# Kernel tuning notes

Hardware: AMD Instinct MI355X
Metric: run time of the kernel (lower is better)

Reference implementation:

```python
import jax, jax.numpy as jnp
import numpy as np

B, C, H, W = 2, 64, 270, 480
CQ = C // 8


def _distance_weight(n):
    i = jnp.arange(n, dtype=jnp.float32)
    d = i[None, :] - i[:, None]  # j - i
    return jnp.exp(-(d * d) / (2.0 * (n * n / 4.0)))  # [n, n]


def setup_inputs() -> dict:
    key = jax.random.key(0)
    ks = jax.random.split(key, 8)
    s = 0.05
    return {
        "x": jax.random.normal(ks[0], (B, C, H, W), jnp.float32),
        "Wq": jax.random.normal(ks[1], (CQ, C), jnp.float32) * s,
        "bq": jax.random.normal(ks[2], (CQ,), jnp.float32) * s,
        "Wk": jax.random.normal(ks[3], (CQ, C), jnp.float32) * s,
        "bk": jax.random.normal(ks[4], (CQ,), jnp.float32) * s,
        "Wv": jax.random.normal(ks[5], (C, C), jnp.float32) * s,
        "bv": jax.random.normal(ks[6], (C,), jnp.float32) * s,
        "gamma": jax.random.normal(ks[7], (), jnp.float32) * 0.3,
        "dw_h": _distance_weight(H),  # [H, H] non-trainable buffer
        "dw_w": _distance_weight(W),  # [W, W] non-trainable buffer
    }


def reference(x, Wq, bq, Wk, bk, Wv, bv, gamma, dw_h, dw_w):
    # 1x1 convs == per-pixel linear projections
    q = jnp.einsum('oc,bchw->bohw', Wq, x) + bq[None, :, None, None]  # [B,CQ,H,W]
    k = jnp.einsum('oc,bchw->bohw', Wk, x) + bk[None, :, None, None]  # [B,CQ,H,W]
    v = jnp.einsum('oc,bchw->bohw', Wv, x) + bv[None, :, None, None]  # [B,C,H,W]

    height, width = x.shape[2], x.shape[3]
    neg_inf = jnp.float32(-jnp.inf)

    # row (H-direction) energy: queries/keys along the height axis per column w
    e_h = jnp.einsum('bchw,bcgw->bwhg', q, k) * dw_h[None, None]  # [B,W,H,H]
    # diagonal -inf mask (dw_h diag == 1, so order of mul is immaterial)
    eye_h = jnp.eye(height, dtype=bool)
    e_h = jnp.where(eye_h[None, None], neg_inf, e_h)
    e_h = jnp.transpose(e_h, (0, 2, 1, 3))  # [B,H,W,H]

    # column (W-direction) energy along the width axis per row h
    e_w = jnp.einsum('bchw,bchv->bhwv', q, k) * dw_w[None, None]  # [B,H,W,W]

    # joint softmax over concatenated H and W directions
    att = jax.nn.softmax(jnp.concatenate([e_h, e_w], axis=3), axis=3)  # [B,H,W,H+W]
    att_h = jnp.transpose(att[:, :, :, :height], (0, 2, 1, 3))  # [B,W,H,H]
    att_w = att[:, :, :, height:]  # [B,H,W,W]

    out_h = jnp.einsum('bcgw,bwhg->bchw', v, att_h)  # [B,C,H,W]
    out_w = jnp.einsum('bchv,bhwv->bchw', v, att_w)  # [B,C,H,W]

    return gamma * (out_h + out_w) + x
```

## Files before the change

### kernel.cpp

```cpp
#include <hip/hip_runtime.h>
#include <hip/hip_bf16.h>

namespace {

constexpr int B  = 2;
constexpr int C  = 64;
constexpr int CQ = 8;
constexpr int H  = 270;
constexpr int W  = 480;
constexpr int HW = H * W;
constexpr float INVH2 = 2.0f / (270.0f * 270.0f);
constexpr float INVW2 = 2.0f / (480.0f * 480.0f);

typedef __attribute__((ext_vector_type(4))) float f32x4;
typedef __attribute__((ext_vector_type(8))) short short8;
typedef __attribute__((ext_vector_type(4))) unsigned int uint4v;

__device__ __forceinline__ float bits2f(unsigned short u) {
  union { unsigned int i; float f; } cv;
  cv.i = ((unsigned int)u) << 16;
  return cv.f;
}

__device__ __forceinline__ unsigned short f2bf(float f) {
  union { __hip_bfloat16 b; unsigned short u; } cv;
  cv.b = __float2bfloat16(f);
  return cv.u;
}

__device__ __forceinline__ unsigned int pack2(float a, float b) {
  return ((unsigned int)f2bf(b) << 16) | (unsigned int)f2bf(a);
}

__device__ __forceinline__ short8 pack_p(const float p0[4], const float p1[4]) {
  uint4v pw;
  pw[0] = pack2(p0[0], p0[1]);
  pw[1] = pack2(p0[2], p0[3]);
  pw[2] = pack2(p1[0], p1[1]);
  pw[3] = pack2(p1[2], p1[3]);
  return __builtin_bit_cast(short8, pw);
}


__global__ __launch_bounds__(256, 1)
void k_qkv(const float* __restrict__ x,
           const float* __restrict__ Wq, const float* __restrict__ bq,
           const float* __restrict__ Wk, const float* __restrict__ bk,
           const float* __restrict__ Wv, const float* __restrict__ bv,
           unsigned short* __restrict__ qwp, unsigned short* __restrict__ kwp,
           unsigned short* __restrict__ qhp, unsigned short* __restrict__ khp,
           unsigned short* __restrict__ v, unsigned short* __restrict__ vt) {
  __shared__ __align__(16) float wql[CQ * C];
  __shared__ __align__(16) float wkl[CQ * C];
  __shared__ __align__(16) float wvl[C * C];
  __shared__ float bql[CQ], bkl[CQ], bvl[C];
  const int tid = threadIdx.x;
  for (int i = tid; i < CQ * C; i += 256) { wql[i] = Wq[i]; wkl[i] = Wk[i]; }
  for (int i = tid; i < C * C; i += 256) wvl[i] = Wv[i];
  if (tid < CQ) { bql[tid] = bq[tid]; bkl[tid] = bk[tid]; }
  if (tid < C) bvl[tid] = bv[tid];
  __syncthreads();
  const int pix0 = (blockIdx.x * 256 + tid) * 2;
  if (pix0 >= B * HW) return;
  const int b = pix0 / HW;
  const int r = pix0 - b * HW;
  const int h = r / W;
  const int w = r - h * W;

  float qa0[CQ], qa1[CQ], ka0[CQ], ka1[CQ], va0[C], va1[C];
#pragma unroll
  for (int o = 0; o < CQ; ++o) {
    qa0[o] = bql[o]; qa1[o] = bql[o];
    ka0[o] = bkl[o]; ka1[o] = bkl[o];
  }
#pragma unroll
  for (int o = 0; o < C; ++o) { va0[o] = bvl[o]; va1[o] = bvl[o]; }

  const float* xp = x + (size_t)b * C * HW + r;
  for (int c = 0; c < C; c += 4) {
    const float2 x0 = *(const float2*)(xp + (size_t)(c + 0) * HW);
    const float2 x1 = *(const float2*)(xp + (size_t)(c + 1) * HW);
    const float2 x2 = *(const float2*)(xp + (size_t)(c + 2) * HW);
    const float2 x3 = *(const float2*)(xp + (size_t)(c + 3) * HW);
#pragma unroll
    for (int o = 0; o < CQ; ++o) {
      const float4 a = *(const float4*)(wql + o * C + c);
      qa0[o] = fmaf(a.w, x3.x, fmaf(a.z, x2.x, fmaf(a.y, x1.x, fmaf(a.x, x0.x, qa0[o]))));
      qa1[o] = fmaf(a.w, x3.y, fmaf(a.z, x2.y, fmaf(a.y, x1.y, fmaf(a.x, x0.y, qa1[o]))));
      const float4 bb = *(const float4*)(wkl + o * C + c);
      ka0[o] = fmaf(bb.w, x3.x, fmaf(bb.z, x2.x, fmaf(bb.y, x1.x, fmaf(bb.x, x0.x, ka0[o]))));
      ka1[o] = fmaf(bb.w, x3.y, fmaf(bb.z, x2.y, fmaf(bb.y, x1.y, fmaf(bb.x, x0.y, ka1[o]))));
    }
#pragma unroll
    for (int o = 0; o < C; ++o) {
      const float4 cc = *(const float4*)(wvl + o * C + c);
      va0[o] = fmaf(cc.w, x3.x, fmaf(cc.z, x2.x, fmaf(cc.y, x1.x, fmaf(cc.x, x0.x, va0[o]))));
      va1[o] = fmaf(cc.w, x3.y, fmaf(cc.z, x2.y, fmaf(cc.y, x1.y, fmaf(cc.x, x0.y, va1[o]))));
    }
  }

  uint4 qp0, kp0, qp1, kp1;
  qp0.x = pack2(qa0[0], qa0[1]); qp0.y = pack2(qa0[2], qa0[3]);
  qp0.z = pack2(qa0[4], qa0[5]); qp0.w = pack2(qa0[6], qa0[7]);
  kp0.x = pack2(ka0[0], ka0[1]); kp0.y = pack2(ka0[2], ka0[3]);
  kp0.z = pack2(ka0[4], ka0[5]); kp0.w = pack2(ka0[6], ka0[7]);
  qp1.x = pack2(qa1[0], qa1[1]); qp1.y = pack2(qa1[2], qa1[3]);
  qp1.z = pack2(qa1[4], qa1[5]); qp1.w = pack2(qa1[6], qa1[7]);
  kp1.x = pack2(ka1[0], ka1[1]); kp1.y = pack2(ka1[2], ka1[3]);
  kp1.z = pack2(ka1[4], ka1[5]); kp1.w = pack2(ka1[6], ka1[7]);
  *(uint4*)(qwp + (size_t)pix0 * 8) = qp0;
  *(uint4*)(qwp + (size_t)(pix0 + 1) * 8) = qp1;
  *(uint4*)(kwp + (size_t)pix0 * 8) = kp0;
  *(uint4*)(kwp + (size_t)(pix0 + 1) * 8) = kp1;
  const size_t tb0 = ((size_t)b * W + w) * H + h;
  const size_t tb1 = tb0 + H;
  *(uint4*)(qhp + tb0 * 8) = qp0;
  *(uint4*)(qhp + tb1 * 8) = qp1;
  *(uint4*)(khp + tb0 * 8) = kp0;
  *(uint4*)(khp + tb1 * 8) = kp1;

  unsigned short* vp = v + (size_t)b * C * HW + r;
#pragma unroll
  for (int o = 0; o < C; ++o)
    *(unsigned int*)(vp + (size_t)o * HW) = pack2(va0[o], va1[o]);
  unsigned short* vt0 = vt + tb0 * C;
  unsigned short* vt1 = vt + tb1 * C;
#pragma unroll
  for (int j = 0; j < 16; ++j) {
    ushort4 u0, u1;
    u0.x = f2bf(va0[4 * j + 0]); u0.y = f2bf(va0[4 * j + 1]);
    u0.z = f2bf(va0[4 * j + 2]); u0.w = f2bf(va0[4 * j + 3]);
    u1.x = f2bf(va1[4 * j + 0]); u1.y = f2bf(va1[4 * j + 1]);
    u1.z = f2bf(va1[4 * j + 2]); u1.w = f2bf(va1[4 * j + 3]);
    *(ushort4*)(vt0 + 4 * j) = u0;
    *(ushort4*)(vt1 + 4 * j) = u1;
  }
}

constexpr int VSW = 494;

__global__ __launch_bounds__(512, 1)
void k_outw(const unsigned short* __restrict__ qwp,
            const unsigned short* __restrict__ kwp,
            const unsigned short* __restrict__ v,
            unsigned short* __restrict__ ow, float* __restrict__ Sw) {
  __shared__ __align__(16) unsigned short vbs[64 * VSW];
  __shared__ __align__(16) unsigned short kls[480 * 8];
  const int h = blockIdx.x >> 1, z = blockIdx.x & 1;
  const int b = blockIdx.y;
  const int tid = threadIdx.x;
  const size_t rowbase = ((size_t)b * H + h) * W;

  const unsigned short* vrow = v + (size_t)b * C * HW + (size_t)h * W;
  ushort4 vr0[8];
#pragma unroll
  for (int it = 0; it < 8; ++it) {
    const int idx = tid + it * 512;
    const int c = idx / 120, s4 = (idx - c * 120) * 4;
    vr0[it] = *(const ushort4*)(vrow + (size_t)c * HW + s4);
  }
  uint4 kreg;
  if (tid < 480) kreg = *(const uint4*)(kwp + (rowbase + tid) * 8);
#pragma unroll
  for (int it = 0; it < 8; ++it) {
    const int idx = tid + it * 512;
    const int c = idx / 120, s4 = (idx - c * 120) * 4;
    const int u = s4 & 31;
    const int t = (u < 16) ? ((u >> 2) * 8) : (((u - 16) >> 2) * 8 + 4);
    *(ushort4*)(vbs + c * VSW + (s4 & ~31) + t) = vr0[it];
  }
  ushort4 vr1[7];
#pragma unroll
  for (int it = 0; it < 7; ++it) {
    const int idx = tid + (8 + it) * 512;
    const int c = idx / 120, s4 = (idx - c * 120) * 4;
    vr1[it] = *(const ushort4*)(vrow + (size_t)c * HW + s4);
  }
#pragma unroll
  for (int it = 0; it < 7; ++it) {
    const int idx = tid + (8 + it) * 512;
    const int c = idx / 120, s4 = (idx - c * 120) * 4;
    const int u = s4 & 31;
    const int t = (u < 16) ? ((u >> 2) * 8) : (((u - 16) >> 2) * 8 + 4);
    *(ushort4*)(vbs + c * VSW + (s4 & ~31) + t) = vr1[it];
  }
  if (tid < 480) *(uint4*)(kls + tid * 8) = kreg;

  const int lane = tid & 63, wv = tid >> 6;
  const int l15 = lane & 15, quad = lane >> 4;
  const int chunk = z * 8 + wv;
  const bool active = chunk < 15;
  const int m0 = chunk * 32;

  short8 qa0 = short8{0, 0, 0, 0, 0, 0, 0, 0};
  short8 qa1 = short8{0, 0, 0, 0, 0, 0, 0, 0};
  if (quad == 0 && active) {
    qa0 = *(const short8*)(qwp + (rowbase + m0 + l15) * 8);
    qa1 = *(const short8*)(qwp + (rowbase + m0 + 16 + l15) * 8);
  }

  f32x4 acc[2][4];
  float Sacc[2] = {0.0f, 0.0f};
#pragma unroll
  for (int mt = 0; mt < 2; ++mt)
#pragma unroll
    for (int ct = 0; ct < 4; ++ct)
#pragma unroll
      for (int rr = 0; rr < 4; ++rr) acc[mt][ct][rr] = 0.0f;

  __syncthreads();

  if (active) {
    short8 kb0 = short8{0, 0, 0, 0, 0, 0, 0, 0};
    short8 kb1 = short8{0, 0, 0, 0, 0, 0, 0, 0};
    if (quad == 0) {
      kb0 = *(const short8*)(kls + (l15) * 8);
      kb1 = *(const short8*)(kls + (16 + l15) * 8);
    }
    for (int ci = 0; ci < 15; ++ci) {
      const int sc = ci * 32;
      short8 nk0 = short8{0, 0, 0, 0, 0, 0, 0, 0};
      short8 nk1 = short8{0, 0, 0, 0, 0, 0, 0, 0};
      if (ci < 14 && quad == 0) {
        nk0 = *(const short8*)(kls + (sc + 32 + l15) * 8);
        nk1 = *(const short8*)(kls + (sc + 48 + l15) * 8);
      }
      short8 vb[4];
#pragma unroll
      for (int ct = 0; ct < 4; ++ct)
        vb[ct] = *(const short8*)(vbs + (ct * 16 + l15) * VSW + sc + quad * 8);
      const f32x4 z4 = f32x4{0.f, 0.f, 0.f, 0.f};
      const f32x4 E00 = __builtin_amdgcn_mfma_f32_16x16x32_bf16(kb0, qa0, z4, 0, 0, 0);
      const f32x4 E01 = __builtin_amdgcn_mfma_f32_16x16x32_bf16(kb1, qa0, z4, 0, 0, 0);
      const f32x4 E10 = __builtin_amdgcn_mfma_f32_16x16x32_bf16(kb0, qa1, z4, 0, 0, 0);
      const f32x4 E11 = __builtin_amdgcn_mfma_f32_16x16x32_bf16(kb1, qa1, z4, 0, 0, 0);
#pragma unroll
      for (int mt = 0; mt < 2; ++mt) {
        const int m = m0 + mt * 16 + l15;
        const f32x4 Ea = mt ? E10 : E00;
        const f32x4 Eb = mt ? E11 : E01;
        float p0[4], p1[4];
#pragma unroll
        for (int rr = 0; rr < 4; ++rr) {
          const float d0 = (float)(m - (sc + quad * 4 + rr));
          const float d1 = d0 - 16.0f;
          p0[rr] = __expf(Ea[rr] * __expf(-(d0 * d0) * INVW2));
          p1[rr] = __expf(Eb[rr] * __expf(-(d1 * d1) * INVW2));
          Sacc[mt] += p0[rr] + p1[rr];
        }
        const short8 pa = pack_p(p0, p1);
#pragma unroll
        for (int ct = 0; ct < 4; ++ct)
          acc[mt][ct] = __builtin_amdgcn_mfma_f32_16x16x32_bf16(pa, vb[ct], acc[mt][ct], 0, 0, 0);
      }
      kb0 = nk0;
      kb1 = nk1;
    }

#pragma unroll
    for (int mt = 0; mt < 2; ++mt) {
      float s = Sacc[mt];
      s += __shfl_xor(s, 16);
      s += __shfl_xor(s, 32);
      if (lane < 16) Sw[rowbase + m0 + mt * 16 + l15] = s;
    }
  }

  __syncthreads();
  unsigned short* ob = vbs;
  if (active) {
#pragma unroll
    for (int mt = 0; mt < 2; ++mt)
#pragma unroll
      for (int ct = 0; ct < 4; ++ct)
#pragma unroll
        for (int rr = 0; rr < 4; ++rr)
          ob[(ct * 16 + l15) * VSW + m0 + mt * 16 + quad * 4 + rr] = f2bf(acc[mt][ct][rr]);
  }
  __syncthreads();
  unsigned short* og = ow + ((size_t)b * H + h) * C * W;
  const int mlo = z ? 256 : 0;
  const int nu = z ? 112 : 128;
  for (int idx = tid; idx < 64 * nu; idx += 512) {
    const int c = idx / nu, i = idx - c * nu;
    *(unsigned int*)(og + (size_t)c * W + mlo + 2 * i) =
        *(const unsigned int*)(ob + c * VSW + mlo + 2 * i);
  }
}

constexpr int VSH = 302;

__global__ __launch_bounds__(576, 1)
void k_outh(const unsigned short* __restrict__ qhp,
            const unsigned short* __restrict__ khp,
            const unsigned short* __restrict__ vt,
            unsigned short* __restrict__ oht, float* __restrict__ Sht) {
  __shared__ __align__(16) unsigned short vbs[64 * VSH];
  __shared__ __align__(16) unsigned short kls[288 * 8];
  const int w = blockIdx.x >> 1, z = blockIdx.x & 1;
  const int b = blockIdx.y;
  const int tid = threadIdx.x;
  const size_t colbase = ((size_t)b * W + w) * H;

  const unsigned short* vtb = vt + colbase * C;
  ushort4 vreg[8];
#pragma unroll
  for (int it = 0; it < 8; ++it) {
    const int idx = tid + it * 576;
    const int g = idx >> 4, c4 = (idx & 15) * 4;
    vreg[it] = (g < H) ? *(const ushort4*)(vtb + (size_t)g * C + c4)
                       : make_ushort4(0, 0, 0, 0);
  }
  uint4 kreg;
  if (tid < 288) kreg = *(const uint4*)(khp + (colbase + min(tid, H - 1)) * 8);
#pragma unroll
  for (int it = 0; it < 8; ++it) {
    const int idx = tid + it * 576;
    const int g = idx >> 4, c4 = (idx & 15) * 4;
    const int u = g & 31;
    const int t = (u < 16) ? ((u >> 2) * 8 + (u & 3))
                           : (((u - 16) >> 2) * 8 + 4 + (u & 3));
    const int slot = (g & ~31) + t;
    vbs[(c4 + 0) * VSH + slot] = vreg[it].x;
    vbs[(c4 + 1) * VSH + slot] = vreg[it].y;
    vbs[(c4 + 2) * VSH + slot] = vreg[it].z;
    vbs[(c4 + 3) * VSH + slot] = vreg[it].w;
  }
  if (tid < 288) *(uint4*)(kls + tid * 8) = kreg;

  const int lane = tid & 63, wv = tid >> 6;
  const int l15 = lane & 15, quad = lane >> 4;
  const int m0 = (z * 9 + wv) * 16;
  const int m = m0 + l15;

  short8 qa = short8{0, 0, 0, 0, 0, 0, 0, 0};
  if (quad == 0)
    qa = *(const short8*)(qhp + (colbase + min(m, H - 1)) * 8);

  f32x4 acc[4];
  float Sacc = 0.0f;
#pragma unroll
  for (int ct = 0; ct < 4; ++ct)
#pragma unroll
    for (int rr = 0; rr < 4; ++rr) acc[ct][rr] = 0.0f;

  __syncthreads();

  for (int ci = 0; ci < 9; ++ci) {
    const int gc = ci * 32;
    short8 kb0 = short8{0, 0, 0, 0, 0, 0, 0, 0};
    short8 kb1 = short8{0, 0, 0, 0, 0, 0, 0, 0};
    if (quad == 0) {
      kb0 = *(const short8*)(kls + (gc + l15) * 8);
      kb1 = *(const short8*)(kls + (gc + 16 + l15) * 8);
    }
    short8 vb[4];
#pragma unroll
    for (int ct = 0; ct < 4; ++ct)
      vb[ct] = *(const short8*)(vbs + (ct * 16 + l15) * VSH + gc + quad * 8);
    const f32x4 z4 = f32x4{0.f, 0.f, 0.f, 0.f};
    const f32x4 E0 = __builtin_amdgcn_mfma_f32_16x16x32_bf16(kb0, qa, z4, 0, 0, 0);
    const f32x4 E1 = __builtin_amdgcn_mfma_f32_16x16x32_bf16(kb1, qa, z4, 0, 0, 0);
    float p0[4], p1[4];
#pragma unroll
    for (int rr = 0; rr < 4; ++rr) {
      const int g0 = gc + quad * 4 + rr;
      const int g1 = g0 + 16;
      const float d0 = (float)(m - g0);
      const float d1 = d0 - 16.0f;
      p0[rr] = (g0 < H && g0 != m)
                   ? __expf(E0[rr] * __expf(-(d0 * d0) * INVH2)) : 0.0f;
      p1[rr] = (g1 < H && g1 != m)
                   ? __expf(E1[rr] * __expf(-(d1 * d1) * INVH2)) : 0.0f;
      Sacc += p0[rr] + p1[rr];
    }
    const short8 pa = pack_p(p0, p1);
#pragma unroll
    for (int ct = 0; ct < 4; ++ct)
      acc[ct] = __builtin_amdgcn_mfma_f32_16x16x32_bf16(pa, vb[ct], acc[ct], 0, 0, 0);
  }

  {
    float s = Sacc;
    s += __shfl_xor(s, 16);
    s += __shfl_xor(s, 32);
    if (lane < 16 && m < H) Sht[colbase + m] = s;
  }

  __syncthreads();
  unsigned short* ob = vbs;
#pragma unroll
  for (int ct = 0; ct < 4; ++ct)
#pragma unroll
    for (int rr = 0; rr < 4; ++rr)
      ob[(ct * 16 + l15) * VSH + m0 + quad * 4 + rr] = f2bf(acc[ct][rr]);
  __syncthreads();
  unsigned short* og = oht + ((size_t)b * W + w) * C * H;
  const int mlo = z ? 144 : 0;
  const int nu = z ? 63 : 72;
  for (int idx = tid; idx < 64 * nu; idx += 576) {
    const int c = idx / nu, i = idx - c * nu;
    *(unsigned int*)(og + (size_t)c * H + mlo + 2 * i) =
        *(const unsigned int*)(ob + c * VSH + mlo + 2 * i);
  }
}

__global__ __launch_bounds__(256)
void k_combine(const unsigned short* __restrict__ oht,
               const unsigned short* __restrict__ ow,
               const float* __restrict__ Sht, const float* __restrict__ Sw,
               const float* __restrict__ x,
               const float* __restrict__ gp,
               float* __restrict__ out) {
  __shared__ float tile[32][33];
  const int b = blockIdx.z >> 6, c = blockIdx.z & 63;
  const int w0 = blockIdx.x * 32, h0 = blockIdx.y * 32;
  const int tx = threadIdx.x, ty = threadIdx.y;
#pragma unroll
  for (int i = 0; i < 4; ++i) {
    const int wl = ty + i * 8;
    const int hh = h0 + tx;
    float val = 0.0f;
    if (hh < H) val = bits2f(oht[(((size_t)b * W + (w0 + wl)) * C + c) * H + hh]);
    tile[wl][tx] = val;
  }
  __syncthreads();
  const float gamma = *gp;
#pragma unroll
  for (int i = 0; i < 4; ++i) {
    const int hl = ty + i * 8;
    const int hh = h0 + hl;
    if (hh < H) {
      const int ww = w0 + tx;
      const float uh = tile[tx][hl];
      const float uw = bits2f(ow[(((size_t)b * H + hh) * C + c) * W + ww]);
      const size_t si = ((size_t)b * H + hh) * W + ww;
      const float Z = Sht[((size_t)b * W + ww) * H + hh] + Sw[si];
      const float invZ = __builtin_amdgcn_rcpf(Z);
      const size_t xi = ((size_t)b * C + c) * HW + (size_t)hh * W + ww;
      out[xi] = fmaf(gamma * invZ, uh + uw, x[xi]);
    }
  }
}

}

extern "C" void kernel_launch(void* const* d_in, const int* in_sizes, int n_in,
                              void* d_out, int out_size, void* d_ws, size_t ws_size,
                              hipStream_t stream) {
  (void)in_sizes; (void)n_in; (void)out_size; (void)ws_size;
  const float* x  = (const float*)d_in[0];
  const float* Wq = (const float*)d_in[1];
  const float* bq = (const float*)d_in[2];
  const float* Wk = (const float*)d_in[3];
  const float* bk = (const float*)d_in[4];
  const float* Wv = (const float*)d_in[5];
  const float* bv = (const float*)d_in[6];
  const float* gp = (const float*)d_in[7];
  float* out = (float*)d_out;

  char* p = (char*)d_ws;
  auto take = [&](size_t bytes) -> void* {
    char* r = p;
    p += (bytes + 255) & ~(size_t)255;
    return (void*)r;
  };
  unsigned short* qwp = (unsigned short*)take(sizeof(unsigned short) * (size_t)B * HW * 8);
  unsigned short* kwp = (unsigned short*)take(sizeof(unsigned short) * (size_t)B * HW * 8);
  unsigned short* qhp = (unsigned short*)take(sizeof(unsigned short) * (size_t)B * HW * 8);
  unsigned short* khp = (unsigned short*)take(sizeof(unsigned short) * (size_t)B * HW * 8);
  unsigned short* v   = (unsigned short*)take(sizeof(unsigned short) * (size_t)B * C * HW);
  unsigned short* vt  = (unsigned short*)take(sizeof(unsigned short) * (size_t)B * C * HW);
  unsigned short* oht = (unsigned short*)take(sizeof(unsigned short) * (size_t)B * C * HW);
  unsigned short* owb = (unsigned short*)take(sizeof(unsigned short) * (size_t)B * C * HW);
  float* Sht = (float*)take(sizeof(float) * (size_t)B * HW);
  float* Sw  = (float*)take(sizeof(float) * (size_t)B * HW);

  hipLaunchKernelGGL(k_qkv, dim3((B * HW / 2 + 255) / 256), dim3(256), 0, stream,
                     x, Wq, bq, Wk, bk, Wv, bv, qwp, kwp, qhp, khp, v, vt);
  hipLaunchKernelGGL(k_outh, dim3(2 * W, B), dim3(576), 0, stream,
                     qhp, khp, vt, oht, Sht);
  hipLaunchKernelGGL(k_outw, dim3(2 * H, B), dim3(512), 0, stream,
                     qwp, kwp, v, owb, Sw);
  hipLaunchKernelGGL(k_combine, dim3(W / 32, (H + 31) / 32, B * C), dim3(32, 8), 0, stream,
                     oht, owb, Sht, Sw, x, gp, out);
}
```

Baseline: 398.8 us.

## Fuse H- and W-direction attention kernels into one launch with interleaved blocks

Merges the separate k_outh and k_outw kernels into a single 640-thread kernel whose grid interleaves row-attention and column-attention blocks. W-direction rows are now split into three blocks of 160 queries, with one 16-query tile per wave instead of two. H-direction columns use 10 waves per half. This removes a kernel boundary and lets the two workloads overlap and balance across CUs. In exchange, both paths now share one shared-memory allocation and one register budget, the W path loses its two-tile K reuse and K prefetch, and some H-path waves sit idle.

New measurement: 516.8 us. 1.3x slower.

```diff
diff --git a/kernel.cpp b/kernel.cpp
--- a/kernel.cpp
+++ b/kernel.cpp
@@ -138,270 +138,248 @@
 }
 
 constexpr int VSW = 494;
-
-__global__ __launch_bounds__(512, 1)
-void k_outw(const unsigned short* __restrict__ qwp,
-            const unsigned short* __restrict__ kwp,
-            const unsigned short* __restrict__ v,
-            unsigned short* __restrict__ ow, float* __restrict__ Sw) {
-  __shared__ __align__(16) unsigned short vbs[64 * VSW];
-  __shared__ __align__(16) unsigned short kls[480 * 8];
-  const int h = blockIdx.x >> 1, z = blockIdx.x & 1;
+constexpr int VSH = 302;
+
+__global__ __launch_bounds__(640, 1)
+void k_att(const unsigned short* __restrict__ qwp,
+           const unsigned short* __restrict__ kwp,
+           const unsigned short* __restrict__ v,
+           unsigned short* __restrict__ ow, float* __restrict__ Sw,
+           const unsigned short* __restrict__ qhp,
+           const unsigned short* __restrict__ khp,
+           const unsigned short* __restrict__ vt,
+           unsigned short* __restrict__ oht, float* __restrict__ Sht) {
+  __shared__ __align__(16) unsigned short smem[64 * VSW + 480 * 8];
   const int b = blockIdx.y;
   const int tid = threadIdx.x;
-  const size_t rowbase = ((size_t)b * H + h) * W;
-
-  const unsigned short* vrow = v + (size_t)b * C * HW + (size_t)h * W;
-  ushort4 vr0[8];
-#pragma unroll
-  for (int it = 0; it < 8; ++it) {
-    const int idx = tid + it * 512;
-    const int c = idx / 120, s4 = (idx - c * 120) * 4;
-    vr0[it] = *(const ushort4*)(vrow + (size_t)c * HW + s4);
-  }
-  uint4 kreg;
-  if (tid < 480) kreg = *(const uint4*)(kwp + (rowbase + tid) * 8);
-#pragma unroll
-  for (int it = 0; it < 8; ++it) {
-    const int idx = tid + it * 512;
-    const int c = idx / 120, s4 = (idx - c * 120) * 4;
-    const int u = s4 & 31;
-    const int t = (u < 16) ? ((u >> 2) * 8) : (((u - 16) >> 2) * 8 + 4);
-    *(ushort4*)(vbs + c * VSW + (s4 & ~31) + t) = vr0[it];
-  }
-  ushort4 vr1[7];
-#pragma unroll
-  for (int it = 0; it < 7; ++it) {
-    const int idx = tid + (8 + it) * 512;
-    const int c = idx / 120, s4 = (idx - c * 120) * 4;
-    vr1[it] = *(const ushort4*)(vrow + (size_t)c * HW + s4);
-  }
-#pragma unroll
-  for (int it = 0; it < 7; ++it) {
-    const int idx = tid + (8 + it) * 512;
-    const int c = idx / 120, s4 = (idx - c * 120) * 4;
-    const int u = s4 & 31;
-    const int t = (u < 16) ? ((u >> 2) * 8) : (((u - 16) >> 2) * 8 + 4);
-    *(ushort4*)(vbs + c * VSW + (s4 & ~31) + t) = vr1[it];
-  }
-  if (tid < 480) *(uint4*)(kls + tid * 8) = kreg;
-
   const int lane = tid & 63, wv = tid >> 6;
   const int l15 = lane & 15, quad = lane >> 4;
-  const int chunk = z * 8 + wv;
-  const bool active = chunk < 15;
-  const int m0 = chunk * 32;
-
-  short8 qa0 = short8{0, 0, 0, 0, 0, 0, 0, 0};
-  short8 qa1 = short8{0, 0, 0, 0, 0, 0, 0, 0};
-  if (quad == 0 && active) {
-    qa0 = *(const short8*)(qwp + (rowbase + m0 + l15) * 8);
-    qa1 = *(const short8*)(qwp + (rowbase + m0 + 16 + l15) * 8);
-  }
-
-  f32x4 acc[2][4];
-  float Sacc[2] = {0.0f, 0.0f};
-#pragma unroll
-  for (int mt = 0; mt < 2; ++mt)
+
+  const int i = blockIdx.x;
+  int part, j;
+  if (i < 1620) { part = i & 1; j = i >> 1; }
+  else          { part = 0;     j = 810 + (i - 1620); }
+
+  if (part == 1) {
+    const int h = j / 3, zz = j - (j / 3) * 3;
+    unsigned short* vbs = smem;
+    unsigned short* kls = smem + 64 * VSW;
+    const size_t rowbase = ((size_t)b * H + h) * W;
+    const unsigned short* vrow = v + (size_t)b * C * HW + (size_t)h * W;
+
+    ushort4 vr[6];
+#pragma unroll
+    for (int it = 0; it < 6; ++it) {
+      const int idx = tid + it * 640;
+      const int c = idx / 120, s4 = (idx - c * 120) * 4;
+      vr[it] = *(const ushort4*)(vrow + (size_t)c * HW + s4);
+    }
+    uint4 kreg;
+    if (tid < 480) kreg = *(const uint4*)(kwp + (rowbase + tid) * 8);
+#pragma unroll
+    for (int it = 0; it < 6; ++it) {
+      const int idx = tid + it * 640;
+      const int c = idx / 120, s4 = (idx - c * 120) * 4;
+      const int u = s4 & 31;
+      const int t = (u < 16) ? ((u >> 2) * 8) : (((u - 16) >> 2) * 8 + 4);
+      *(ushort4*)(vbs + c * VSW + (s4 & ~31) + t) = vr[it];
+    }
+#pragma unroll
+    for (int it = 0; it < 6; ++it) {
+      const int idx = tid + (6 + it) * 640;
+      const int c = idx / 120, s4 = (idx - c * 120) * 4;
+      vr[it] = *(const ushort4*)(vrow + (size_t)c * HW + s4);
+    }
+#pragma unroll
+    for (int it = 0; it < 6; ++it) {
+      const int idx = tid + (6 + it) * 640;
+      const int c = idx / 120, s4 = (idx - c * 120) * 4;
+      const int u = s4 & 31;
+      const int t = (u < 16) ? ((u >> 2) * 8) : (((u - 16) >> 2) * 8 + 4);
+      *(ushort4*)(vbs + c * VSW + (s4 & ~31) + t) = vr[it];
+    }
+    if (tid < 480) *(uint4*)(kls + tid * 8) = kreg;
+
+    const int m0 = (zz * 10 + wv) * 16;
+    const int m = m0 + l15;
+
+    short8 qa = short8{0, 0, 0, 0, 0, 0, 0, 0};
+    if (quad == 0) qa = *(const short8*)(qwp + (rowbase + m) * 8);
+
+    f32x4 acc[4];
+    float Sacc = 0.0f;
 #pragma unroll
     for (int ct = 0; ct < 4; ++ct)
 #pragma unroll
-      for (int rr = 0; rr < 4; ++rr) acc[mt][ct][rr] = 0.0f;
-
-  __syncthreads();
-
-  if (active) {
-    short8 kb0 = short8{0, 0, 0, 0, 0, 0, 0, 0};
-    short8 kb1 = short8{0, 0, 0, 0, 0, 0, 0, 0};
-    if (quad == 0) {
-      kb0 = *(const short8*)(kls + (l15) * 8);
-      kb1 = *(const short8*)(kls + (16 + l15) * 8);
-    }
+      for (int rr = 0; rr < 4; ++rr) acc[ct][rr] = 0.0f;
+
+    __syncthreads();
+
     for (int ci = 0; ci < 15; ++ci) {
       const int sc = ci * 32;
-      short8 nk0 = short8{0, 0, 0, 0, 0, 0, 0, 0};
-      short8 nk1 = short8{0, 0, 0, 0, 0, 0, 0, 0};
-      if (ci < 14 && quad == 0) {
-        nk0 = *(const short8*)(kls + (sc + 32 + l15) * 8);
-        nk1 = *(const short8*)(kls + (sc + 48 + l15) * 8);
+      short8 kb0 = short8{0, 0, 0, 0, 0, 0, 0, 0};
+      short8 kb1 = short8{0, 0, 0, 0, 0, 0, 0, 0};
+      if (quad == 0) {
+        kb0 = *(const short8*)(kls + (sc + l15) * 8);
+        kb1 = *(const short8*)(kls + (sc + 16 + l15) * 8);
       }
       short8 vb[4];
 #pragma unroll
       for (int ct = 0; ct < 4; ++ct)
         vb[ct] = *(const short8*)(vbs + (ct * 16 + l15) * VSW + sc + quad * 8);
       const f32x4 z4 = f32x4{0.f, 0.f, 0.f, 0.f};
-      const f32x4 E00 = __builtin_amdgcn_mfma_f32_16x16x32_bf16(kb0, qa0, z4, 0, 0, 0);
-      const f32x4 E01 = __builtin_amdgcn_mfma_f32_16x16x32_bf16(kb1, qa0, z4, 0, 0, 0);
-      const f32x4 E10 = __builtin_amdgcn_mfma_f32_16x16x32_bf16(kb0, qa1, z4, 0, 0, 0);
-      const f32x4 E11 = __builtin_amdgcn_mfma_f32_16x16x32_bf16(kb1, qa1, z4, 0, 0, 0);
-#pragma unroll
-      for (int mt = 0; mt < 2; ++mt) {
-        const int m = m0 + mt * 16 + l15;
-        const f32x4 Ea = mt ? E10 : E00;
-        const f32x4 Eb = mt ? E11 : E01;
+      const f32x4 E0 = __builtin_amdgcn_mfma_f32_16x16x32_bf16(kb0, qa, z4, 0, 0, 0);
+      const f32x4 E1 = __builtin_amdgcn_mfma_f32_16x16x32_bf16(kb1, qa, z4, 0, 0, 0);
+      float p0[4], p1[4];
+#pragma unroll
+      for (int rr = 0; rr < 4; ++rr) {
+        const float d0 = (float)(m - (sc + quad * 4 + rr));
+        const float d1 = d0 - 16.0f;
+        p0[rr] = __expf(E0[rr] * __expf(-(d0 * d0) * INVW2));
+        p1[rr] = __expf(E1[rr] * __expf(-(d1 * d1) * INVW2));
+        Sacc += p0[rr] + p1[rr];
+      }
+      const short8 pa = pack_p(p0, p1);
+#pragma unroll
+      for (int ct = 0; ct < 4; ++ct)
+        acc[ct] = __builtin_amdgcn_mfma_f32_16x16x32_bf16(pa, vb[ct], acc[ct], 0, 0, 0);
+    }
+
+    {
+      float s = Sacc;
+      s += __shfl_xor(s, 16);
+      s += __shfl_xor(s, 32);
+      if (lane < 16) Sw[rowbase + m] = s;
+    }
+
+    __syncthreads();
+    unsigned short* ob = vbs;
+#pragma unroll
+    for (int ct = 0; ct < 4; ++ct)
+#pragma unroll
+      for (int rr = 0; rr < 4; ++rr)
+        ob[(ct * 16 + l15) * VSW + m0 + quad * 4 + rr] = f2bf(acc[ct][rr]);
+    __syncthreads();
+    unsigned short* og = ow + ((size_t)b * H + h) * C * W;
+    const int mlo = zz * 160;
+    for (int idx = tid; idx < 64 * 80; idx += 640) {
+      const int c = idx / 80, i2 = idx - c * 80;
+      *(unsigned int*)(og + (size_t)c * W + mlo + 2 * i2) =
+          *(const unsigned int*)(ob + c * VSW + mlo + 2 * i2);
+    }
+  } else {
+    const int w = j >> 1, z = j & 1;
+    unsigned short* vbs = smem;
+    unsigned short* kls = smem + 64 * VSH;
+    const size_t colbase = ((size_t)b * W + w) * H;
+    const unsigned short* vtb = vt + colbase * C;
+
+    ushort4 vreg[8];
+#pragma unroll
+    for (int it = 0; it < 8; ++it) {
+      const int idx = tid + it * 640;
+      if (idx < 4608) {
+        const int g = idx >> 4, c4 = (idx & 15) * 4;
+        vreg[it] = (g < H) ? *(const ushort4*)(vtb + (size_t)g * C + c4)
+                           : make_ushort4(0, 0, 0, 0);
+      }
+    }
+    uint4 kreg;
+    if (tid < 288) kreg = *(const uint4*)(khp + (colbase + min(tid, H - 1)) * 8);
+#pragma unroll
+    for (int it = 0; it < 8; ++it) {
+      const int idx = tid + it * 640;
+      if (idx < 4608) {
+        const int g = idx >> 4, c4 = (idx & 15) * 4;
+        const int u = g & 31;
+        const int t = (u < 16) ? ((u >> 2) * 8 + (u & 3))
+                               : (((u - 16) >> 2) * 8 + 4 + (u & 3));
+        const int slot = (g & ~31) + t;
+        vbs[(c4 + 0) * VSH + slot] = vreg[it].x;
+        vbs[(c4 + 1) * VSH + slot] = vreg[it].y;
+        vbs[(c4 + 2) * VSH + slot] = vreg[it].z;
+        vbs[(c4 + 3) * VSH + slot] = vreg[it].w;
+      }
+    }
+    if (tid < 288) *(uint4*)(kls + tid * 8) = kreg;
+
+    const int chunk = z * 10 + wv;
+    const bool active = chunk < 18;
+    const int m0 = chunk * 16;
+    const int m = m0 + l15;
+
+    short8 qa = short8{0, 0, 0, 0, 0, 0, 0, 0};
+    if (quad == 0 && active)
+      qa = *(const short8*)(qhp + (colbase + min(m, H - 1)) * 8);
+
+    f32x4 acc[4];
+    float Sacc = 0.0f;
+#pragma unroll
+    for (int ct = 0; ct < 4; ++ct)
+#pragma unroll
+      for (int rr = 0; rr < 4; ++rr) acc[ct][rr] = 0.0f;
+
+    __syncthreads();
+
+    if (active) {
+      for (int ci = 0; ci < 9; ++ci) {
+        const int gc = ci * 32;
+        short8 kb0 = short8{0, 0, 0, 0, 0, 0, 0, 0};
+        short8 kb1 = short8{0, 0, 0, 0, 0, 0, 0, 0};
+        if (quad == 0) {
+          kb0 = *(const short8*)(kls + (gc + l15) * 8);
+          kb1 = *(const short8*)(kls + (gc + 16 + l15) * 8);
+        }
+        short8 vb[4];
+#pragma unroll
+        for (int ct = 0; ct < 4; ++ct)
+          vb[ct] = *(const short8*)(vbs + (ct * 16 + l15) * VSH + gc + quad * 8);
+        const f32x4 z4 = f32x4{0.f, 0.f, 0.f, 0.f};
+        const f32x4 E0 = __builtin_amdgcn_mfma_f32_16x16x32_bf16(kb0, qa, z4, 0, 0, 0);
+        const f32x4 E1 = __builtin_amdgcn_mfma_f32_16x16x32_bf16(kb1, qa, z4, 0, 0, 0);
         float p0[4], p1[4];
 #pragma unroll
         for (int rr = 0; rr < 4; ++rr) {
-          const float d0 = (float)(m - (sc + quad * 4 + rr));
+          const int g0 = gc + quad * 4 + rr;
+          const int g1 = g0 + 16;
+          const float d0 = (float)(m - g0);
           const float d1 = d0 - 16.0f;
-          p0[rr] = __expf(Ea[rr] * __expf(-(d0 * d0) * INVW2));
-          p1[rr] = __expf(Eb[rr] * __expf(-(d1 * d1) * INVW2));
-          Sacc[mt] += p0[rr] + p1[rr];
+          p0[rr] = (g0 < H && g0 != m)
+                       ? __expf(E0[rr] * __expf(-(d0 * d0) * INVH2)) : 0.0f;
+          p1[rr] = (g1 < H && g1 != m)
+                       ? __expf(E1[rr] * __expf(-(d1 * d1) * INVH2)) : 0.0f;
+          Sacc += p0[rr] + p1[rr];
         }
         const short8 pa = pack_p(p0, p1);
 #pragma unroll
         for (int ct = 0; ct < 4; ++ct)
-          acc[mt][ct] = __builtin_amdgcn_mfma_f32_16x16x32_bf16(pa, vb[ct], acc[mt][ct], 0, 0, 0);
+          acc[ct] = __builtin_amdgcn_mfma_f32_16x16x32_bf16(pa, vb[ct], acc[ct], 0, 0, 0);
       }
-      kb0 = nk0;
-      kb1 = nk1;
-    }
-
-#pragma unroll
-    for (int mt = 0; mt < 2; ++mt) {
-      float s = Sacc[mt];
+
+      float s = Sacc;
       s += __shfl_xor(s, 16);
       s += __shfl_xor(s, 32);
-      if (lane < 16) Sw[rowbase + m0 + mt * 16 + l15] = s;
-    }
-  }
-
-  __syncthreads();
-  unsigned short* ob = vbs;
-  if (active) {
-#pragma unroll
-    for (int mt = 0; mt < 2; ++mt)
+      if (lane < 16 && m < H) Sht[colbase + m] = s;
+    }
+
+    __syncthreads();
+    unsigned short* ob = vbs;
+    if (active) {
 #pragma unroll
       for (int ct = 0; ct < 4; ++ct)
 #pragma unroll
         for (int rr = 0; rr < 4; ++rr)
-          ob[(ct * 16 + l15) * VSW + m0 + mt * 16 + quad * 4 + rr] = f2bf(acc[mt][ct][rr]);
-  }
-  __syncthreads();
-  unsigned short* og = ow + ((size_t)b * H + h) * C * W;
-  const int mlo = z ? 256 : 0;
-  const int nu = z ? 112 : 128;
-  for (int idx = tid; idx < 64 * nu; idx += 512) {
-    const int c = idx / nu, i = idx - c * nu;
-    *(unsigned int*)(og + (size_t)c * W + mlo + 2 * i) =
-        *(const unsigned int*)(ob + c * VSW + mlo + 2 * i);
-  }
-}
-
-constexpr int VSH = 302;
-
-__global__ __launch_bounds__(576, 1)
-void k_outh(const unsigned short* __restrict__ qhp,
-            const unsigned short* __restrict__ khp,
-            const unsigned short* __restrict__ vt,
-            unsigned short* __restrict__ oht, float* __restrict__ Sht) {
-  __shared__ __align__(16) unsigned short vbs[64 * VSH];
-  __shared__ __align__(16) unsigned short kls[288 * 8];
-  const int w = blockIdx.x >> 1, z = blockIdx.x & 1;
-  const int b = blockIdx.y;
-  const int tid = threadIdx.x;
-  const size_t colbase = ((size_t)b * W + w) * H;
-
-  const unsigned short* vtb = vt + colbase * C;
-  ushort4 vreg[8];
-#pragma unroll
-  for (int it = 0; it < 8; ++it) {
-    const int idx = tid + it * 576;
-    const int g = idx >> 4, c4 = (idx & 15) * 4;
-    vreg[it] = (g < H) ? *(const ushort4*)(vtb + (size_t)g * C + c4)
-                       : make_ushort4(0, 0, 0, 0);
-  }
-  uint4 kreg;
-  if (tid < 288) kreg = *(const uint4*)(khp + (colbase + min(tid, H - 1)) * 8);
-#pragma unroll
-  for (int it = 0; it < 8; ++it) {
-    const int idx = tid + it * 576;
-    const int g = idx >> 4, c4 = (idx & 15) * 4;
-    const int u = g & 31;
-    const int t = (u < 16) ? ((u >> 2) * 8 + (u & 3))
-                           : (((u - 16) >> 2) * 8 + 4 + (u & 3));
-    const int slot = (g & ~31) + t;
-    vbs[(c4 + 0) * VSH + slot] = vreg[it].x;
-    vbs[(c4 + 1) * VSH + slot] = vreg[it].y;
-    vbs[(c4 + 2) * VSH + slot] = vreg[it].z;
-    vbs[(c4 + 3) * VSH + slot] = vreg[it].w;
-  }
-  if (tid < 288) *(uint4*)(kls + tid * 8) = kreg;
-
-  const int lane = tid & 63, wv = tid >> 6;
-  const int l15 = lane & 15, quad = lane >> 4;
-  const int m0 = (z * 9 + wv) * 16;
-  const int m = m0 + l15;
-
-  short8 qa = short8{0, 0, 0, 0, 0, 0, 0, 0};
-  if (quad == 0)
-    qa = *(const short8*)(qhp + (colbase + min(m, H - 1)) * 8);
-
-  f32x4 acc[4];
-  float Sacc = 0.0f;
-#pragma unroll
-  for (int ct = 0; ct < 4; ++ct)
-#pragma unroll
-    for (int rr = 0; rr < 4; ++rr) acc[ct][rr] = 0.0f;
-
-  __syncthreads();
-
-  for (int ci = 0; ci < 9; ++ci) {
-    const int gc = ci * 32;
-    short8 kb0 = short8{0, 0, 0, 0, 0, 0, 0, 0};
-    short8 kb1 = short8{0, 0, 0, 0, 0, 0, 0, 0};
-    if (quad == 0) {
-      kb0 = *(const short8*)(kls + (gc + l15) * 8);
-      kb1 = *(const short8*)(kls + (gc + 16 + l15) * 8);
-    }
-    short8 vb[4];
-#pragma unroll
-    for (int ct = 0; ct < 4; ++ct)
-      vb[ct] = *(const short8*)(vbs + (ct * 16 + l15) * VSH + gc + quad * 8);
-    const f32x4 z4 = f32x4{0.f, 0.f, 0.f, 0.f};
-    const f32x4 E0 = __builtin_amdgcn_mfma_f32_16x16x32_bf16(kb0, qa, z4, 0, 0, 0);
-    const f32x4 E1 = __builtin_amdgcn_mfma_f32_16x16x32_bf16(kb1, qa, z4, 0, 0, 0);
-    float p0[4], p1[4];
-#pragma unroll
-    for (int rr = 0; rr < 4; ++rr) {
-      const int g0 = gc + quad * 4 + rr;
-      const int g1 = g0 + 16;
-      const float d0 = (float)(m - g0);
-      const float d1 = d0 - 16.0f;
-      p0[rr] = (g0 < H && g0 != m)
-                   ? __expf(E0[rr] * __expf(-(d0 * d0) * INVH2)) : 0.0f;
-      p1[rr] = (g1 < H && g1 != m)
-                   ? __expf(E1[rr] * __expf(-(d1 * d1) * INVH2)) : 0.0f;
-      Sacc += p0[rr] + p1[rr];
-    }
-    const short8 pa = pack_p(p0, p1);
-#pragma unroll
-    for (int ct = 0; ct < 4; ++ct)
-      acc[ct] = __builtin_amdgcn_mfma_f32_16x16x32_bf16(pa, vb[ct], acc[ct], 0, 0, 0);
-  }
-
-  {
-    float s = Sacc;
-    s += __shfl_xor(s, 16);
-    s += __shfl_xor(s, 32);
-    if (lane < 16 && m < H) Sht[colbase + m] = s;
-  }
-
-  __syncthreads();
-  unsigned short* ob = vbs;
-#pragma unroll
-  for (int ct = 0; ct < 4; ++ct)
-#pragma unroll
-    for (int rr = 0; rr < 4; ++rr)
-      ob[(ct * 16 + l15) * VSH + m0 + quad * 4 + rr] = f2bf(acc[ct][rr]);
-  __syncthreads();
-  unsigned short* og = oht + ((size_t)b * W + w) * C * H;
-  const int mlo = z ? 144 : 0;
-  const int nu = z ? 63 : 72;
-  for (int idx = tid; idx < 64 * nu; idx += 576) {
-    const int c = idx / nu, i = idx - c * nu;
-    *(unsigned int*)(og + (size_t)c * H + mlo + 2 * i) =
-        *(const unsigned int*)(ob + c * VSH + mlo + 2 * i);
+          ob[(ct * 16 + l15) * VSH + m0 + quad * 4 + rr] = f2bf(acc[ct][rr]);
+    }
+    __syncthreads();
+    unsigned short* og = oht + ((size_t)b * W + w) * C * H;
+    const int mlo = z ? 160 : 0;
+    const int nu = z ? 55 : 80;
+    for (int idx = tid; idx < 64 * nu; idx += 640) {
+      const int c = idx / nu, i2 = idx - c * nu;
+      *(unsigned int*)(og + (size_t)c * H + mlo + 2 * i2) =
+          *(const unsigned int*)(ob + c * VSH + mlo + 2 * i2);
+    }
   }
 }
 
@@ -478,10 +456,8 @@
 
   hipLaunchKernelGGL(k_qkv, dim3((B * HW / 2 + 255) / 256), dim3(256), 0, stream,
                      x, Wq, bq, Wk, bk, Wv, bv, qwp, kwp, qhp, khp, v, vt);
-  hipLaunchKernelGGL(k_outh, dim3(2 * W, B), dim3(576), 0, stream,
-                     qhp, khp, vt, oht, Sht);
-  hipLaunchKernelGGL(k_outw, dim3(2 * H, B), dim3(512), 0, stream,
-                     qwp, kwp, v, owb, Sw);
+  hipLaunchKernelGGL(k_att, dim3(2 * W + 3 * H, B), dim3(640), 0, stream,
+                     qwp, kwp, v, owb, Sw, qhp, khp, vt, oht, Sht);
   hipLaunchKernelGGL(k_combine, dim3(W / 32, (H + 31) / 32, B * C), dim3(32, 8), 0, stream,
                      oht, owb, Sht, Sw, x, gp, out);
 }
```
